# Optimization experiments

Measured on AMD Instinct MI355X. Metric: run time of the kernel, lower is better.

## Reference

```python
import jax, jax.numpy as jnp
import numpy as np

SEQ = 4096
HIDDEN = 4096
HEAD_DIM = 1024
NUM_HEAD = HIDDEN // HEAD_DIM  # 4


def setup_inputs() -> dict:
    key = jax.random.key(0)
    ks = jax.random.split(key, 7)
    scale = 1.0 / np.sqrt(HIDDEN)  # torch Linear default-ish init scale
    h = jax.random.normal(ks[0], (SEQ, HIDDEN), dtype=jnp.float32)
    Wq = jax.random.normal(ks[1], (NUM_HEAD, HIDDEN, HEAD_DIM), dtype=jnp.float32) * scale
    bq = jax.random.normal(ks[2], (NUM_HEAD, HEAD_DIM), dtype=jnp.float32) * scale
    Wk = jax.random.normal(ks[3], (NUM_HEAD, HIDDEN, HEAD_DIM), dtype=jnp.float32) * scale
    bk = jax.random.normal(ks[4], (NUM_HEAD, HEAD_DIM), dtype=jnp.float32) * scale
    Wv = jax.random.normal(ks[5], (NUM_HEAD, HIDDEN, HEAD_DIM), dtype=jnp.float32) * scale
    bv = jax.random.normal(ks[6], (NUM_HEAD, HEAD_DIM), dtype=jnp.float32) * scale
    return {"h": h, "Wq": Wq, "bq": bq, "Wk": Wk, "bk": bk, "Wv": Wv, "bv": bv}


def reference(h, Wq, bq, Wk, bk, Wv, bv):
    # Batched per-head projections: q/k/v [H, S, E]
    q = jnp.einsum('sd,hde->hse', h, Wq) + bq[:, None, :]
    k = jnp.einsum('sd,hde->hse', h, Wk) + bk[:, None, :]
    v = jnp.einsum('sd,hde->hse', h, Wv) + bv[:, None, :]
    # Full (non-causal) attention scores [H, S, S], scaled by sqrt(head_dim)
    s = jnp.einsum('hse,hte->hst', q, k) / jnp.sqrt(jnp.asarray(HEAD_DIM, h.dtype))
    p = jax.nn.softmax(s, axis=-1)
    out = jnp.einsum('hst,hte->hse', p, v)  # [H, S, E]
    # Concatenate heads along feature dim -> [S, H*E]
    return jnp.transpose(out, (1, 0, 2)).reshape(h.shape[0], -1)
```

## Files before the change

### kernel.cpp

```cpp
#include <hip/hip_runtime.h>

#define SEQ   4096
#define HID   4096
#define EDIM  1024
#define NHEAD 4

typedef __attribute__((ext_vector_type(8))) short short8;
typedef __attribute__((ext_vector_type(4))) float f32x4;

typedef const __attribute__((address_space(1))) void* gas_ptr;
typedef __attribute__((address_space(3))) void* las_ptr;
#define GLD16(g, l) __builtin_amdgcn_global_load_lds((gas_ptr)(g), (las_ptr)(l), 16, 0, 0)

#define BARRIER() __builtin_amdgcn_s_barrier()
#define SCHED0()  __builtin_amdgcn_sched_barrier(0)

__device__ __forceinline__ unsigned short f2bf(float f) {
  union { float f; unsigned u; } v; v.f = f;
  unsigned r = v.u + 0x7fffu + ((v.u >> 16) & 1u);
  return (unsigned short)(r >> 16);
}
__device__ __forceinline__ float bf2f(unsigned short u) {
  union { unsigned u; float f; } v; v.u = ((unsigned)u) << 16;
  return v.f;
}

__global__ __launch_bounds__(256) void hconv_kernel(const float* __restrict__ in,
                                                    unsigned short* __restrict__ out) {
  size_t i = ((size_t)blockIdx.x * 256 + threadIdx.x) * 8;
  const float4 a = *(const float4*)(in + i);
  const float4 b = *(const float4*)(in + i + 4);
  short8 o;
  o[0] = (short)f2bf(a.x); o[1] = (short)f2bf(a.y);
  o[2] = (short)f2bf(a.z); o[3] = (short)f2bf(a.w);
  o[4] = (short)f2bf(b.x); o[5] = (short)f2bf(b.y);
  o[6] = (short)f2bf(b.z); o[7] = (short)f2bf(b.w);
  *(short8*)(out + i) = o;
}

__global__ __launch_bounds__(256) void wconv_kernel(const float* __restrict__ Wq,
                                                    const float* __restrict__ Wk,
                                                    const float* __restrict__ Wv,
                                                    unsigned short* __restrict__ wt) {
  const int mh = blockIdx.y;
  const int mat = mh >> 2, head = mh & 3;
  const float* W = (mat == 0 ? Wq : (mat == 1 ? Wk : Wv)) + (size_t)head * HID * EDIM;
  unsigned short* out = wt + (size_t)mh * EDIM * HID;
  const int tile = blockIdx.x;
  const int td = tile >> 4;
  const int te = tile & 15;
  __shared__ float lds[64][65];
  const int tid = threadIdx.x;
  const int r = tid >> 4, c4 = (tid & 15) * 4;
#pragma unroll
  for (int it = 0; it < 4; ++it) {
    int dr = r + 16 * it;
    const float4 v = *(const float4*)&W[(size_t)(td * 64 + dr) * EDIM + te * 64 + c4];
    lds[dr][c4 + 0] = v.x; lds[dr][c4 + 1] = v.y;
    lds[dr][c4 + 2] = v.z; lds[dr][c4 + 3] = v.w;
  }
  __syncthreads();
#pragma unroll
  for (int it = 0; it < 4; ++it) {
    int er = r + 16 * it;
    ushort4 o;
    o.x = f2bf(lds[c4 + 0][er]); o.y = f2bf(lds[c4 + 1][er]);
    o.z = f2bf(lds[c4 + 2][er]); o.w = f2bf(lds[c4 + 3][er]);
    *(ushort4*)&out[(size_t)(te * 64 + er) * HID + td * 64 + c4] = o;
  }
}

template <int MODE>
__global__ __launch_bounds__(512, 2) void gemm256_kernel(
    const unsigned short* __restrict__ Aall, const unsigned short* __restrict__ Ball,
    long long aBatch, long long bBatch, int K,
    const float* __restrict__ biasAll, long long biasBatch,
    void* __restrict__ outAll, long long outBatch, int ldOut, float scale,
    int gx, int gxy) {
  extern __shared__ char smem[];

  const int nwg = (int)gridDim.x;
  const int lin = (int)blockIdx.x;
  int wg = (lin & 7) * (nwg >> 3) + (lin >> 3);
  const int z = wg / gxy; wg -= z * gxy;
  const int by = wg / gx;
  const int bx = wg - by * gx;
  const int bm = by * 256, bn = bx * 256;

  const unsigned short* A = Aall + (size_t)z * aBatch;
  const unsigned short* B = Ball + (size_t)z * bBatch;

  const int tid = threadIdx.x;
  const int lane = tid & 63, wid = tid >> 6;
  const int wr = wid >> 2, wc = wid & 3;
  const int li = lane & 15, lg = lane >> 4;

  const int srow = tid >> 3;
  const int sk = ((tid & 7) ^ (srow & 7)) * 8;
  const unsigned short* aS00 = A + (size_t)(bm +   0 + srow) * K + sk;
  const unsigned short* aS01 = A + (size_t)(bm +  64 + srow) * K + sk;
  const unsigned short* aS10 = A + (size_t)(bm + 128 + srow) * K + sk;
  const unsigned short* aS11 = A + (size_t)(bm + 192 + srow) * K + sk;
  const unsigned short* bS00 = B + (size_t)(bn +   0 + srow) * K + sk;
  const unsigned short* bS01 = B + (size_t)(bn +  64 + srow) * K + sk;
  const unsigned short* bS10 = B + (size_t)(bn + 128 + srow) * K + sk;
  const unsigned short* bS11 = B + (size_t)(bn + 192 + srow) * K + sk;

#define STG(p0, p1, regionOff, tt)                                        \
  do {                                                                    \
    char* _d = smem + (((tt) & 1) << 16) + (regionOff) + tid * 16;        \
    GLD16((p0) + (size_t)(tt) * 64, _d);                                  \
    GLD16((p1) + (size_t)(tt) * 64, _d + 8192);                           \
  } while (0)

  const int aBase = (wr * 128 + li) * 128;
  const int bBase = 32768 + (wc * 64 + li) * 128;
  const int axk0 = ((0 + lg) ^ (li & 7)) * 16;
  const int axk1 = ((4 + lg) ^ (li & 7)) * 16;

  f32x4 acc[8][4];
#pragma unroll
  for (int m = 0; m < 8; ++m)
#pragma unroll
    for (int n = 0; n < 4; ++n) acc[m][n] = (f32x4){0.f, 0.f, 0.f, 0.f};

  const int NT = K >> 6;
  const int NI = NT >> 1;

  STG(aS00, aS01, 0, 0);
  STG(aS10, aS11, 16384, 0);
  STG(bS00, bS01, 32768, 0);
  STG(bS10, bS11, 49152, 0);
  STG(bS00, bS01, 32768, 1);
  STG(bS10, bS11, 49152, 1);
  asm volatile("s_waitcnt vmcnt(4)" ::: "memory");
  BARRIER();
  SCHED0();

  short8 av[4][2], bv[4][2];

  for (int i = 0; i < NI; ++i) {
    const int t = 2 * i;
    const char* s0 = smem;
    const char* s1 = smem + 65536;

#pragma unroll
    for (int m = 0; m < 4; ++m) {
      av[m][0] = *(const short8*)(s0 + aBase + m * 2048 + axk0);
      av[m][1] = *(const short8*)(s0 + aBase + m * 2048 + axk1);
    }
#pragma unroll
    for (int n = 0; n < 2; ++n) {
      bv[n][0] = *(const short8*)(s0 + bBase + n * 2048 + axk0);
      bv[n][1] = *(const short8*)(s0 + bBase + n * 2048 + axk1);
    }
    STG(aS00, aS01, 0, t + 1);
    asm volatile("s_waitcnt lgkmcnt(8)" ::: "memory");
    SCHED0();
    BARRIER();
    asm volatile("s_waitcnt lgkmcnt(0)" ::: "memory");
    SCHED0();
    __builtin_amdgcn_s_setprio(1);
#pragma unroll
    for (int m = 0; m < 4; ++m)
#pragma unroll
      for (int n = 0; n < 2; ++n) {
        acc[m][n] = __builtin_amdgcn_mfma_f32_16x16x32_bf16(av[m][0], bv[n][0], acc[m][n], 0, 0, 0);
        acc[m][n] = __builtin_amdgcn_mfma_f32_16x16x32_bf16(av[m][1], bv[n][1], acc[m][n], 0, 0, 0);
      }
    __builtin_amdgcn_s_setprio(0);
    SCHED0();
    BARRIER();

#pragma unroll
    for (int n = 2; n < 4; ++n) {
      bv[n][0] = *(const short8*)(s0 + bBase + n * 2048 + axk0);
      bv[n][1] = *(const short8*)(s0 + bBase + n * 2048 + axk1);
    }
    STG(aS10, aS11, 16384, t + 1);
    SCHED0();
    BARRIER();
    asm volatile("s_waitcnt lgkmcnt(0)" ::: "memory");
    SCHED0();
    __builtin_amdgcn_s_setprio(1);
#pragma unroll
    for (int m = 0; m < 4; ++m)
#pragma unroll
      for (int n = 2; n < 4; ++n) {
        acc[m][n] = __builtin_amdgcn_mfma_f32_16x16x32_bf16(av[m][0], bv[n][0], acc[m][n], 0, 0, 0);
        acc[m][n] = __builtin_amdgcn_mfma_f32_16x16x32_bf16(av[m][1], bv[n][1], acc[m][n], 0, 0, 0);
      }
    __builtin_amdgcn_s_setprio(0);
    SCHED0();
    BARRIER();

#pragma unroll
    for (int m = 0; m < 4; ++m) {
      av[m][0] = *(const short8*)(s0 + aBase + (m + 4) * 2048 + axk0);
      av[m][1] = *(const short8*)(s0 + aBase + (m + 4) * 2048 + axk1);
    }
    if (t + 2 < NT) STG(bS00, bS01, 32768, t + 2);
    SCHED0();
    BARRIER();
    asm volatile("s_waitcnt lgkmcnt(0)" ::: "memory");
    SCHED0();
    __builtin_amdgcn_s_setprio(1);
#pragma unroll
    for (int m = 0; m < 4; ++m)
#pragma unroll
      for (int n = 0; n < 2; ++n) {
        acc[m + 4][n] = __builtin_amdgcn_mfma_f32_16x16x32_bf16(av[m][0], bv[n][0], acc[m + 4][n], 0, 0, 0);
        acc[m + 4][n] = __builtin_amdgcn_mfma_f32_16x16x32_bf16(av[m][1], bv[n][1], acc[m + 4][n], 0, 0, 0);
      }
    __builtin_amdgcn_s_setprio(0);
    SCHED0();
    BARRIER();

    if (t + 2 < NT) {
      STG(bS10, bS11, 49152, t + 2);
      asm volatile("s_waitcnt vmcnt(4)" ::: "memory");
    } else {
      asm volatile("s_waitcnt vmcnt(0)" ::: "memory");
    }
    SCHED0();
    BARRIER();
    __builtin_amdgcn_s_setprio(1);
#pragma unroll
    for (int m = 0; m < 4; ++m)
#pragma unroll
      for (int n = 2; n < 4; ++n) {
        acc[m + 4][n] = __builtin_amdgcn_mfma_f32_16x16x32_bf16(av[m][0], bv[n][0], acc[m + 4][n], 0, 0, 0);
        acc[m + 4][n] = __builtin_amdgcn_mfma_f32_16x16x32_bf16(av[m][1], bv[n][1], acc[m + 4][n], 0, 0, 0);
      }
    __builtin_amdgcn_s_setprio(0);
    SCHED0();
    BARRIER();

#pragma unroll
    for (int m = 0; m < 4; ++m) {
      av[m][0] = *(const short8*)(s1 + aBase + m * 2048 + axk0);
      av[m][1] = *(const short8*)(s1 + aBase + m * 2048 + axk1);
    }
#pragma unroll
    for (int n = 0; n < 2; ++n) {
      bv[n][0] = *(const short8*)(s1 + bBase + n * 2048 + axk0);
      bv[n][1] = *(const short8*)(s1 + bBase + n * 2048 + axk1);
    }
    if (t + 2 < NT) STG(aS00, aS01, 0, t + 2);
    asm volatile("s_waitcnt lgkmcnt(8)" ::: "memory");
    SCHED0();
    BARRIER();
    asm volatile("s_waitcnt lgkmcnt(0)" ::: "memory");
    SCHED0();
    __builtin_amdgcn_s_setprio(1);
#pragma unroll
    for (int m = 0; m < 4; ++m)
#pragma unroll
      for (int n = 0; n < 2; ++n) {
        acc[m][n] = __builtin_amdgcn_mfma_f32_16x16x32_bf16(av[m][0], bv[n][0], acc[m][n], 0, 0, 0);
        acc[m][n] = __builtin_amdgcn_mfma_f32_16x16x32_bf16(av[m][1], bv[n][1], acc[m][n], 0, 0, 0);
      }
    __builtin_amdgcn_s_setprio(0);
    SCHED0();
    BARRIER();

#pragma unroll
    for (int n = 2; n < 4; ++n) {
      bv[n][0] = *(const short8*)(s1 + bBase + n * 2048 + axk0);
      bv[n][1] = *(const short8*)(s1 + bBase + n * 2048 + axk1);
    }
    if (t + 2 < NT) STG(aS10, aS11, 16384, t + 2);
    SCHED0();
    BARRIER();
    asm volatile("s_waitcnt lgkmcnt(0)" ::: "memory");
    SCHED0();
    __builtin_amdgcn_s_setprio(1);
#pragma unroll
    for (int m = 0; m < 4; ++m)
#pragma unroll
      for (int n = 2; n < 4; ++n) {
        acc[m][n] = __builtin_amdgcn_mfma_f32_16x16x32_bf16(av[m][0], bv[n][0], acc[m][n], 0, 0, 0);
        acc[m][n] = __builtin_amdgcn_mfma_f32_16x16x32_bf16(av[m][1], bv[n][1], acc[m][n], 0, 0, 0);
      }
    __builtin_amdgcn_s_setprio(0);
    SCHED0();
    BARRIER();

#pragma unroll
    for (int m = 0; m < 4; ++m) {
      av[m][0] = *(const short8*)(s1 + aBase + (m + 4) * 2048 + axk0);
      av[m][1] = *(const short8*)(s1 + aBase + (m + 4) * 2048 + axk1);
    }
    if (t + 3 < NT) STG(bS00, bS01, 32768, t + 3);
    SCHED0();
    BARRIER();
    asm volatile("s_waitcnt lgkmcnt(0)" ::: "memory");
    SCHED0();
    __builtin_amdgcn_s_setprio(1);
#pragma unroll
    for (int m = 0; m < 4; ++m)
#pragma unroll
      for (int n = 0; n < 2; ++n) {
        acc[m + 4][n] = __builtin_amdgcn_mfma_f32_16x16x32_bf16(av[m][0], bv[n][0], acc[m + 4][n], 0, 0, 0);
        acc[m + 4][n] = __builtin_amdgcn_mfma_f32_16x16x32_bf16(av[m][1], bv[n][1], acc[m + 4][n], 0, 0, 0);
      }
    __builtin_amdgcn_s_setprio(0);
    SCHED0();
    BARRIER();

    if (t + 3 < NT) {
      STG(bS10, bS11, 49152, t + 3);
      asm volatile("s_waitcnt vmcnt(4)" ::: "memory");
    } else {
      asm volatile("s_waitcnt vmcnt(0)" ::: "memory");
    }
    SCHED0();
    BARRIER();
    __builtin_amdgcn_s_setprio(1);
#pragma unroll
    for (int m = 0; m < 4; ++m)
#pragma unroll
      for (int n = 2; n < 4; ++n) {
        acc[m + 4][n] = __builtin_amdgcn_mfma_f32_16x16x32_bf16(av[m][0], bv[n][0], acc[m + 4][n], 0, 0, 0);
        acc[m + 4][n] = __builtin_amdgcn_mfma_f32_16x16x32_bf16(av[m][1], bv[n][1], acc[m + 4][n], 0, 0, 0);
      }
    __builtin_amdgcn_s_setprio(0);
    SCHED0();
    BARRIER();
  }
#undef STG

  float bvv[4];
  if (MODE == 0 || MODE == 1) {
    const float* bias = biasAll + (size_t)z * biasBatch;
#pragma unroll
    for (int n = 0; n < 4; ++n) bvv[n] = bias[bn + wc * 64 + n * 16 + li];
  }
#pragma unroll
  for (int m = 0; m < 8; ++m)
#pragma unroll
    for (int n = 0; n < 4; ++n)
#pragma unroll
      for (int r = 0; r < 4; ++r) {
        const int grow = bm + wr * 128 + m * 16 + lg * 4 + r;
        const int gcol = bn + wc * 64 + n * 16 + li;
        float val = acc[m][n][r];
        if (MODE == 0 || MODE == 1) val += bvv[n];
        if (MODE == 2) val *= scale;
        if (MODE == 0 || MODE == 2) {
          unsigned short* o = (unsigned short*)outAll + (size_t)z * outBatch;
          o[(size_t)grow * ldOut + gcol] = f2bf(val);
        } else if (MODE == 1) {
          unsigned short* o = (unsigned short*)outAll + (size_t)z * outBatch;
          o[(size_t)gcol * ldOut + grow] = f2bf(val);
        } else {
          float* o = (float*)outAll + (size_t)z * outBatch;
          o[(size_t)grow * ldOut + gcol] = val;
        }
      }
}

__global__ __launch_bounds__(256) void softmax_kernel(unsigned short* __restrict__ Sb) {
  const size_t row = blockIdx.x;
  unsigned short* p = Sb + row * (size_t)SEQ;
  const int tid = threadIdx.x;
  const int lane = tid & 63, wid = tid >> 6;
  float v[16];
  const short8 u0 = *(const short8*)&p[tid * 16];
  const short8 u1 = *(const short8*)&p[tid * 16 + 8];
#pragma unroll
  for (int j = 0; j < 8; ++j) v[j] = bf2f((unsigned short)u0[j]);
#pragma unroll
  for (int j = 0; j < 8; ++j) v[8 + j] = bf2f((unsigned short)u1[j]);
  float mx = v[0];
#pragma unroll
  for (int j = 1; j < 16; ++j) mx = fmaxf(mx, v[j]);
#pragma unroll
  for (int off = 32; off; off >>= 1) mx = fmaxf(mx, __shfl_xor(mx, off));
  __shared__ float red[8];
  if (lane == 0) red[wid] = mx;
  __syncthreads();
  mx = fmaxf(fmaxf(red[0], red[1]), fmaxf(red[2], red[3]));
  float s = 0.f;
#pragma unroll
  for (int j = 0; j < 16; ++j) { v[j] = __expf(v[j] - mx); s += v[j]; }
#pragma unroll
  for (int off = 32; off; off >>= 1) s += __shfl_xor(s, off);
  if (lane == 0) red[4 + wid] = s;
  __syncthreads();
  s = (red[4] + red[5]) + (red[6] + red[7]);
  const float inv = 1.0f / s;
  short8 o0, o1;
#pragma unroll
  for (int j = 0; j < 8; ++j) o0[j] = (short)f2bf(v[j] * inv);
#pragma unroll
  for (int j = 0; j < 8; ++j) o1[j] = (short)f2bf(v[8 + j] * inv);
  *(short8*)&p[tid * 16] = o0;
  *(short8*)&p[tid * 16 + 8] = o1;
}

extern "C" void kernel_launch(void* const* d_in, const int* in_sizes, int n_in,
                              void* d_out, int out_size, void* d_ws, size_t ws_size,
                              hipStream_t stream) {
  const float* h  = (const float*)d_in[0];
  const float* Wq = (const float*)d_in[1];
  const float* bq = (const float*)d_in[2];
  const float* Wk = (const float*)d_in[3];
  const float* bk = (const float*)d_in[4];
  const float* Wv = (const float*)d_in[5];
  const float* bv = (const float*)d_in[6];
  float* out = (float*)d_out;
  char* ws = (char*)d_ws;

  (void)hipFuncSetAttribute((const void*)&gemm256_kernel<0>,
                            hipFuncAttributeMaxDynamicSharedMemorySize, 131072);
  (void)hipFuncSetAttribute((const void*)&gemm256_kernel<1>,
                            hipFuncAttributeMaxDynamicSharedMemorySize, 131072);
  (void)hipFuncSetAttribute((const void*)&gemm256_kernel<2>,
                            hipFuncAttributeMaxDynamicSharedMemorySize, 131072);
  (void)hipFuncSetAttribute((const void*)&gemm256_kernel<3>,
                            hipFuncAttributeMaxDynamicSharedMemorySize, 131072);

  unsigned short* hB = (unsigned short*)ws;
  unsigned short* wt = (unsigned short*)(ws + (32ull << 20));
  unsigned short* Sb = (unsigned short*)ws;
  unsigned short* Qb = (unsigned short*)(ws + (128ull << 20));
  unsigned short* Kb = (unsigned short*)(ws + (160ull << 20));
  unsigned short* Vt = (unsigned short*)(ws + (192ull << 20));

  const long long WED = (long long)EDIM * HID;
  const long long QKB = (long long)SEQ * EDIM;
  const long long SSB = (long long)SEQ * SEQ;

  hconv_kernel<<<dim3((SEQ * (size_t)HID) / (256 * 8)), 256, 0, stream>>>(h, hB);
  wconv_kernel<<<dim3((HID / 64) * (EDIM / 64), 12), 256, 0, stream>>>(Wq, Wk, Wv, wt);

  gemm256_kernel<0><<<dim3(4 * 16 * 4), 512, 131072, stream>>>(
      hB, wt + 0 * WED, 0, WED, HID, bq, EDIM, Qb, QKB, EDIM, 1.f, 4, 64);
  gemm256_kernel<0><<<dim3(4 * 16 * 4), 512, 131072, stream>>>(
      hB, wt + 4 * WED, 0, WED, HID, bk, EDIM, Kb, QKB, EDIM, 1.f, 4, 64);
  gemm256_kernel<1><<<dim3(4 * 16 * 4), 512, 131072, stream>>>(
      hB, wt + 8 * WED, 0, WED, HID, bv, EDIM, Vt, QKB, SEQ, 1.f, 4, 64);

  gemm256_kernel<2><<<dim3(16 * 16 * 4), 512, 131072, stream>>>(
      Qb, Kb, QKB, QKB, EDIM, nullptr, 0, Sb, SSB, SEQ, 0.03125f, 16, 256);

  softmax_kernel<<<dim3(NHEAD * SEQ), 256, 0, stream>>>(Sb);

  gemm256_kernel<3><<<dim3(4 * 16 * 4), 512, 131072, stream>>>(
      Sb, Vt, SSB, QKB, SEQ, nullptr, 0, out, (long long)EDIM, NHEAD * EDIM, 1.f, 4, 64);
}
```

Baseline: 717.0 us.

## Software-pipeline LDS fragment reads ahead of MFMA quadrants in GEMM main loop

```diff
diff --git a/kernel.cpp b/kernel.cpp
--- a/kernel.cpp
+++ b/kernel.cpp
@@ -127,208 +127,170 @@
   const int NT = K >> 6;
   const int NI = NT >> 1;
 
+  short8 avL[4][2], avH[4][2], bvL[2][2], bvH[2][2];
+
+#define RD_AVL(S)                                                          \
+  _Pragma("unroll") for (int m = 0; m < 4; ++m) {                          \
+    avL[m][0] = *(const short8*)((S) + aBase + m * 2048 + axk0);           \
+    avL[m][1] = *(const short8*)((S) + aBase + m * 2048 + axk1);           \
+  }
+#define RD_AVH(S)                                                          \
+  _Pragma("unroll") for (int m = 0; m < 4; ++m) {                          \
+    avH[m][0] = *(const short8*)((S) + aBase + (m + 4) * 2048 + axk0);     \
+    avH[m][1] = *(const short8*)((S) + aBase + (m + 4) * 2048 + axk1);     \
+  }
+#define RD_BVL(S)                                                          \
+  _Pragma("unroll") for (int n = 0; n < 2; ++n) {                          \
+    bvL[n][0] = *(const short8*)((S) + bBase + n * 2048 + axk0);           \
+    bvL[n][1] = *(const short8*)((S) + bBase + n * 2048 + axk1);           \
+  }
+#define RD_BVH(S)                                                          \
+  _Pragma("unroll") for (int n = 0; n < 2; ++n) {                          \
+    bvH[n][0] = *(const short8*)((S) + bBase + (n + 2) * 2048 + axk0);     \
+    bvH[n][1] = *(const short8*)((S) + bBase + (n + 2) * 2048 + axk1);     \
+  }
+#define MFMA_Q(AV, BV, MO, NO)                                             \
+  _Pragma("unroll") for (int m = 0; m < 4; ++m)                            \
+  _Pragma("unroll") for (int n = 0; n < 2; ++n) {                          \
+    acc[m + MO][n + NO] = __builtin_amdgcn_mfma_f32_16x16x32_bf16(         \
+        AV[m][0], BV[n][0], acc[m + MO][n + NO], 0, 0, 0);                 \
+    acc[m + MO][n + NO] = __builtin_amdgcn_mfma_f32_16x16x32_bf16(         \
+        AV[m][1], BV[n][1], acc[m + MO][n + NO], 0, 0, 0);                 \
+  }
+#define LGKM(N) asm volatile("s_waitcnt lgkmcnt(" #N ")" ::: "memory")
+#define VMC(N)  asm volatile("s_waitcnt vmcnt(" #N ")" ::: "memory")
+
   STG(aS00, aS01, 0, 0);
   STG(aS10, aS11, 16384, 0);
   STG(bS00, bS01, 32768, 0);
   STG(bS10, bS11, 49152, 0);
   STG(bS00, bS01, 32768, 1);
   STG(bS10, bS11, 49152, 1);
-  asm volatile("s_waitcnt vmcnt(4)" ::: "memory");
+  VMC(4);
   BARRIER();
   SCHED0();
-
-  short8 av[4][2], bv[4][2];
+  RD_AVL(smem); RD_BVL(smem);
+  SCHED0();
 
   for (int i = 0; i < NI; ++i) {
     const int t = 2 * i;
     const char* s0 = smem;
     const char* s1 = smem + 65536;
 
-#pragma unroll
-    for (int m = 0; m < 4; ++m) {
-      av[m][0] = *(const short8*)(s0 + aBase + m * 2048 + axk0);
-      av[m][1] = *(const short8*)(s0 + aBase + m * 2048 + axk1);
-    }
-#pragma unroll
-    for (int n = 0; n < 2; ++n) {
-      bv[n][0] = *(const short8*)(s0 + bBase + n * 2048 + axk0);
-      bv[n][1] = *(const short8*)(s0 + bBase + n * 2048 + axk1);
-    }
+    RD_BVH(s0);
+    SCHED0();
     STG(aS00, aS01, 0, t + 1);
-    asm volatile("s_waitcnt lgkmcnt(8)" ::: "memory");
-    SCHED0();
-    BARRIER();
-    asm volatile("s_waitcnt lgkmcnt(0)" ::: "memory");
-    SCHED0();
-    __builtin_amdgcn_s_setprio(1);
-#pragma unroll
-    for (int m = 0; m < 4; ++m)
-#pragma unroll
-      for (int n = 0; n < 2; ++n) {
-        acc[m][n] = __builtin_amdgcn_mfma_f32_16x16x32_bf16(av[m][0], bv[n][0], acc[m][n], 0, 0, 0);
-        acc[m][n] = __builtin_amdgcn_mfma_f32_16x16x32_bf16(av[m][1], bv[n][1], acc[m][n], 0, 0, 0);
-      }
-    __builtin_amdgcn_s_setprio(0);
-    SCHED0();
-    BARRIER();
-
-#pragma unroll
-    for (int n = 2; n < 4; ++n) {
-      bv[n][0] = *(const short8*)(s0 + bBase + n * 2048 + axk0);
-      bv[n][1] = *(const short8*)(s0 + bBase + n * 2048 + axk1);
-    }
+    LGKM(4);
+    SCHED0();
+    __builtin_amdgcn_s_setprio(1);
+    MFMA_Q(avL, bvL, 0, 0);
+    __builtin_amdgcn_s_setprio(0);
+    SCHED0();
+    BARRIER();
+    SCHED0();
+
+    RD_AVH(s0);
+    SCHED0();
     STG(aS10, aS11, 16384, t + 1);
-    SCHED0();
-    BARRIER();
-    asm volatile("s_waitcnt lgkmcnt(0)" ::: "memory");
-    SCHED0();
-    __builtin_amdgcn_s_setprio(1);
-#pragma unroll
-    for (int m = 0; m < 4; ++m)
-#pragma unroll
-      for (int n = 2; n < 4; ++n) {
-        acc[m][n] = __builtin_amdgcn_mfma_f32_16x16x32_bf16(av[m][0], bv[n][0], acc[m][n], 0, 0, 0);
-        acc[m][n] = __builtin_amdgcn_mfma_f32_16x16x32_bf16(av[m][1], bv[n][1], acc[m][n], 0, 0, 0);
-      }
-    __builtin_amdgcn_s_setprio(0);
-    SCHED0();
-    BARRIER();
-
-#pragma unroll
-    for (int m = 0; m < 4; ++m) {
-      av[m][0] = *(const short8*)(s0 + aBase + (m + 4) * 2048 + axk0);
-      av[m][1] = *(const short8*)(s0 + aBase + (m + 4) * 2048 + axk1);
-    }
+    LGKM(8);
+    SCHED0();
+    __builtin_amdgcn_s_setprio(1);
+    MFMA_Q(avL, bvH, 0, 2);
+    __builtin_amdgcn_s_setprio(0);
+    SCHED0();
+    BARRIER();
+    SCHED0();
+
     if (t + 2 < NT) STG(bS00, bS01, 32768, t + 2);
-    SCHED0();
-    BARRIER();
-    asm volatile("s_waitcnt lgkmcnt(0)" ::: "memory");
-    SCHED0();
-    __builtin_amdgcn_s_setprio(1);
-#pragma unroll
-    for (int m = 0; m < 4; ++m)
-#pragma unroll
-      for (int n = 0; n < 2; ++n) {
-        acc[m + 4][n] = __builtin_amdgcn_mfma_f32_16x16x32_bf16(av[m][0], bv[n][0], acc[m + 4][n], 0, 0, 0);
-        acc[m + 4][n] = __builtin_amdgcn_mfma_f32_16x16x32_bf16(av[m][1], bv[n][1], acc[m + 4][n], 0, 0, 0);
-      }
-    __builtin_amdgcn_s_setprio(0);
-    SCHED0();
-    BARRIER();
+    LGKM(0);
+    SCHED0();
+    __builtin_amdgcn_s_setprio(1);
+    MFMA_Q(avH, bvL, 4, 0);
+    __builtin_amdgcn_s_setprio(0);
+    SCHED0();
+    BARRIER();
+    SCHED0();
 
     if (t + 2 < NT) {
       STG(bS10, bS11, 49152, t + 2);
-      asm volatile("s_waitcnt vmcnt(4)" ::: "memory");
+      VMC(4);
     } else {
-      asm volatile("s_waitcnt vmcnt(0)" ::: "memory");
+      VMC(0);
     }
     SCHED0();
     BARRIER();
-    __builtin_amdgcn_s_setprio(1);
-#pragma unroll
-    for (int m = 0; m < 4; ++m)
-#pragma unroll
-      for (int n = 2; n < 4; ++n) {
-        acc[m + 4][n] = __builtin_amdgcn_mfma_f32_16x16x32_bf16(av[m][0], bv[n][0], acc[m + 4][n], 0, 0, 0);
-        acc[m + 4][n] = __builtin_amdgcn_mfma_f32_16x16x32_bf16(av[m][1], bv[n][1], acc[m + 4][n], 0, 0, 0);
-      }
-    __builtin_amdgcn_s_setprio(0);
-    SCHED0();
-    BARRIER();
-
-#pragma unroll
-    for (int m = 0; m < 4; ++m) {
-      av[m][0] = *(const short8*)(s1 + aBase + m * 2048 + axk0);
-      av[m][1] = *(const short8*)(s1 + aBase + m * 2048 + axk1);
-    }
-#pragma unroll
-    for (int n = 0; n < 2; ++n) {
-      bv[n][0] = *(const short8*)(s1 + bBase + n * 2048 + axk0);
-      bv[n][1] = *(const short8*)(s1 + bBase + n * 2048 + axk1);
-    }
+    SCHED0();
+    RD_AVL(s1); RD_BVL(s1);
+    SCHED0();
+    __builtin_amdgcn_s_setprio(1);
+    MFMA_Q(avH, bvH, 4, 2);
+    __builtin_amdgcn_s_setprio(0);
+    SCHED0();
+    BARRIER();
+    SCHED0();
+
+    RD_BVH(s1);
+    SCHED0();
     if (t + 2 < NT) STG(aS00, aS01, 0, t + 2);
-    asm volatile("s_waitcnt lgkmcnt(8)" ::: "memory");
-    SCHED0();
-    BARRIER();
-    asm volatile("s_waitcnt lgkmcnt(0)" ::: "memory");
-    SCHED0();
-    __builtin_amdgcn_s_setprio(1);
-#pragma unroll
-    for (int m = 0; m < 4; ++m)
-#pragma unroll
-      for (int n = 0; n < 2; ++n) {
-        acc[m][n] = __builtin_amdgcn_mfma_f32_16x16x32_bf16(av[m][0], bv[n][0], acc[m][n], 0, 0, 0);
-        acc[m][n] = __builtin_amdgcn_mfma_f32_16x16x32_bf16(av[m][1], bv[n][1], acc[m][n], 0, 0, 0);
-      }
-    __builtin_amdgcn_s_setprio(0);
-    SCHED0();
-    BARRIER();
-
-#pragma unroll
-    for (int n = 2; n < 4; ++n) {
-      bv[n][0] = *(const short8*)(s1 + bBase + n * 2048 + axk0);
-      bv[n][1] = *(const short8*)(s1 + bBase + n * 2048 + axk1);
-    }
+    LGKM(4);
+    SCHED0();
+    __builtin_amdgcn_s_setprio(1);
+    MFMA_Q(avL, bvL, 0, 0);
+    __builtin_amdgcn_s_setprio(0);
+    SCHED0();
+    BARRIER();
+    SCHED0();
+
+    RD_AVH(s1);
+    SCHED0();
     if (t + 2 < NT) STG(aS10, aS11, 16384, t + 2);
-    SCHED0();
-    BARRIER();
-    asm volatile("s_waitcnt lgkmcnt(0)" ::: "memory");
-    SCHED0();
-    __builtin_amdgcn_s_setprio(1);
-#pragma unroll
-    for (int m = 0; m < 4; ++m)
-#pragma unroll
-      for (int n = 2; n < 4; ++n) {
-        acc[m][n] = __builtin_amdgcn_mfma_f32_16x16x32_bf16(av[m][0], bv[n][0], acc[m][n], 0, 0, 0);
-        acc[m][n] = __builtin_amdgcn_mfma_f32_16x16x32_bf16(av[m][1], bv[n][1], acc[m][n], 0, 0, 0);
-      }
-    __builtin_amdgcn_s_setprio(0);
-    SCHED0();
-    BARRIER();
-
-#pragma unroll
-    for (int m = 0; m < 4; ++m) {
-      av[m][0] = *(const short8*)(s1 + aBase + (m + 4) * 2048 + axk0);
-      av[m][1] = *(const short8*)(s1 + aBase + (m + 4) * 2048 + axk1);
-    }
+    LGKM(8);
+    SCHED0();
+    __builtin_amdgcn_s_setprio(1);
+    MFMA_Q(avL, bvH, 0, 2);
+    __builtin_amdgcn_s_setprio(0);
+    SCHED0();
+    BARRIER();
+    SCHED0();
+
     if (t + 3 < NT) STG(bS00, bS01, 32768, t + 3);
-    SCHED0();
-    BARRIER();
-    asm volatile("s_waitcnt lgkmcnt(0)" ::: "memory");
-    SCHED0();
-    __builtin_amdgcn_s_setprio(1);
-#pragma unroll
-    for (int m = 0; m < 4; ++m)
-#pragma unroll
-      for (int n = 0; n < 2; ++n) {
-        acc[m + 4][n] = __builtin_amdgcn_mfma_f32_16x16x32_bf16(av[m][0], bv[n][0], acc[m + 4][n], 0, 0, 0);
-        acc[m + 4][n] = __builtin_amdgcn_mfma_f32_16x16x32_bf16(av[m][1], bv[n][1], acc[m + 4][n], 0, 0, 0);
-      }
-    __builtin_amdgcn_s_setprio(0);
-    SCHED0();
-    BARRIER();
+    LGKM(0);
+    SCHED0();
+    __builtin_amdgcn_s_setprio(1);
+    MFMA_Q(avH, bvL, 4, 0);
+    __builtin_amdgcn_s_setprio(0);
+    SCHED0();
+    BARRIER();
+    SCHED0();
 
     if (t + 3 < NT) {
       STG(bS10, bS11, 49152, t + 3);
-      asm volatile("s_waitcnt vmcnt(4)" ::: "memory");
+      VMC(4);
     } else {
-      asm volatile("s_waitcnt vmcnt(0)" ::: "memory");
+      VMC(0);
     }
     SCHED0();
     BARRIER();
-    __builtin_amdgcn_s_setprio(1);
-#pragma unroll
-    for (int m = 0; m < 4; ++m)
-#pragma unroll
-      for (int n = 2; n < 4; ++n) {
-        acc[m + 4][n] = __builtin_amdgcn_mfma_f32_16x16x32_bf16(av[m][0], bv[n][0], acc[m + 4][n], 0, 0, 0);
-        acc[m + 4][n] = __builtin_amdgcn_mfma_f32_16x16x32_bf16(av[m][1], bv[n][1], acc[m + 4][n], 0, 0, 0);
-      }
-    __builtin_amdgcn_s_setprio(0);
-    SCHED0();
-    BARRIER();
+    SCHED0();
+    if (i + 1 < NI) {
+      RD_AVL(s0); RD_BVL(s0);
+    }
+    SCHED0();
+    __builtin_amdgcn_s_setprio(1);
+    MFMA_Q(avH, bvH, 4, 2);
+    __builtin_amdgcn_s_setprio(0);
+    SCHED0();
+    BARRIER();
+    SCHED0();
   }
 #undef STG
+#undef RD_AVL
+#undef RD_AVH
+#undef RD_BVL
+#undef RD_BVH
+#undef MFMA_Q
+#undef LGKM
+#undef VMC
 
   float bvv[4];
   if (MODE == 0 || MODE == 1) {
```

Measured after the change: 1.179 ms. 64.4% more time.
